# Performance work log

Measured on AMD Instinct MI355X. Metric: run time of the kernel, lower is better.

## Reference

```python
import jax, jax.numpy as jnp
import numpy as np

NODE_SIZE = 100000
DIM = 512
B = 2048
GAMMA = 3.0
LAMB = 20.0
TAU = 8.0


def setup_inputs() -> dict:
    key = jax.random.key(0)
    k1, k2 = jax.random.split(key)
    pairs = jax.random.randint(k1, (B, 2), 0, NODE_SIZE, dtype=jnp.int64 if jax.config.jax_enable_x64 else jnp.int32)
    emb = jax.random.normal(k2, (NODE_SIZE, DIM), dtype=jnp.float32)
    return {"pairs": pairs, "emb": emb}


def _align_loss(pairs, emb):
    l = pairs[:, 0]
    r = pairs[:, 1]
    l_emb = emb[l]                     # [B, D]
    r_emb = emb[r]                     # [B, D]
    pos_dis = jnp.sum(jnp.square(l_emb - r_emb), axis=-1, keepdims=True)  # [B, 1]

    emb_sq = jnp.sum(jnp.square(emb), axis=1)          # [N]

    def squared_dist(A):
        # ||a||^2 + ||b||^2 - 2 a.b  -> [B, N]
        a_sq = jnp.sum(jnp.square(A), axis=1, keepdims=True)
        return a_sq + emb_sq[None, :] - 2.0 * (A @ emb.T)

    l_neg_dis = squared_dist(l_emb)
    r_neg_dis = squared_dist(r_emb)

    # mask = 1 - one_hot(l) - one_hot(r), built without materializing one-hots
    rows = jnp.arange(B)
    mask = jnp.ones((B, NODE_SIZE), dtype=emb.dtype)
    mask = mask.at[rows, l].add(-1.0)
    mask = mask.at[rows, r].add(-1.0)

    def norm_lse(loss):
        loss = loss * mask
        mu = jax.lax.stop_gradient(jnp.mean(loss, axis=-1, keepdims=True))
        sd = jax.lax.stop_gradient(jnp.std(loss, axis=-1, keepdims=True))  # unbiased=False
        loss = (loss - mu) / sd
        return jax.scipy.special.logsumexp(LAMB * loss + TAU, axis=-1)

    l_loss = norm_lse(pos_dis - l_neg_dis + GAMMA)
    r_loss = norm_lse(pos_dis - r_neg_dis + GAMMA)
    return jnp.mean(l_loss + r_loss)


def reference(pairs, emb):
    return _align_loss(pairs, emb)
```

## Files before the change

kernel.cpp:

```cpp
#include <hip/hip_runtime.h>
#include <stdint.h>

#define NODES   100000
#define NPAD    100096
#define DIM     512
#define NPAIR   2048
#define MROWS   4096
#define NB      782
#define GAMMA_F 3.0f
#define LAMB_F  20.0f
#define TAU_F   8.0f
#define SHIFT_F 140.0f

#define TM 128
#define TN 128
#define BK 64

typedef __attribute__((ext_vector_type(8))) short          short8;
typedef __attribute__((ext_vector_type(8))) unsigned short ushort8;
typedef __attribute__((ext_vector_type(4))) float          f32x4;


__device__ __forceinline__ unsigned short f2bf(float f) {
    unsigned u = __float_as_uint(f);
    u += 0x7FFFu + ((u >> 16) & 1u);
    return (unsigned short)(u >> 16);
}
__device__ __forceinline__ float bf2f(unsigned short h) {
    return __uint_as_float(((unsigned)h) << 16);
}

__device__ __forceinline__ void gload_lds16(const void* g, void* l) {
    unsigned lofs = (unsigned)__builtin_amdgcn_readfirstlane((unsigned)(uintptr_t)l);
    auto lp = reinterpret_cast<__attribute__((address_space(3))) unsigned*>(lofs);
    auto gp = (const __attribute__((address_space(1))) unsigned*)g;
    __builtin_amdgcn_global_load_lds(gp, lp, 16, 0, 0);
}


__global__ void convert_stats_kernel(const float* __restrict__ emb,
                                     unsigned short* __restrict__ Ebf,
                                     float* __restrict__ esq,
                                     float* __restrict__ Spart,
                                     float* __restrict__ Tpart,
                                     float* __restrict__ E1part,
                                     float* __restrict__ E2part) {
    __shared__ float Sl[4][512];
    __shared__ float Tl[4][512];
    __shared__ float ew[8];
    const int b = blockIdx.x, t = threadIdx.x;
    const int lane = t & 63, wave = t >> 6;
    const int r0 = b * 196;
    float sacc[8], tacc[8];
    #pragma unroll
    for (int k = 0; k < 8; ++k) { sacc[k] = 0.f; tacc[k] = 0.f; }
    float e1 = 0.f, e2 = 0.f;
    for (int i = 0; i < 49; ++i) {
        const int row = r0 + i * 4 + wave;
        if (row >= NPAD) continue;
        const bool real = row < NODES;
        float v[8];
        float ss = 0.f;
        if (real) {
            const float4* p = (const float4*)(emb + (size_t)row * DIM + lane * 8);
            float4 a = p[0], bb = p[1];
            v[0]=a.x; v[1]=a.y; v[2]=a.z; v[3]=a.w;
            v[4]=bb.x; v[5]=bb.y; v[6]=bb.z; v[7]=bb.w;
            #pragma unroll
            for (int k = 0; k < 8; ++k) ss += v[k] * v[k];
        } else {
            #pragma unroll
            for (int k = 0; k < 8; ++k) v[k] = 0.f;
        }
        #pragma unroll
        for (int o = 1; o < 64; o <<= 1) ss += __shfl_xor(ss, o);
        ushort8 o8;
        float vr[8];
        #pragma unroll
        for (int k = 0; k < 8; ++k) { o8[k] = f2bf(v[k]); vr[k] = bf2f(o8[k]); }
        *(ushort8*)(Ebf + (size_t)row * DIM + lane * 8) = o8;
        if (lane == 0) esq[row] = ss;
        if (real) {
            #pragma unroll
            for (int k = 0; k < 8; ++k) { sacc[k] += vr[k]; tacc[k] += ss * vr[k]; }
            if (lane == 0) { e1 += ss; e2 += ss * ss; }
        }
    }
    #pragma unroll
    for (int k = 0; k < 8; ++k) {
        Sl[wave][lane * 8 + k] = sacc[k];
        Tl[wave][lane * 8 + k] = tacc[k];
    }
    if (lane == 0) { ew[wave] = e1; ew[4 + wave] = e2; }
    __syncthreads();
    #pragma unroll
    for (int kk = 0; kk < 2; ++kk) {
        const int d = 2 * t + kk;
        Spart[(size_t)b * 512 + d] = Sl[0][d] + Sl[1][d] + Sl[2][d] + Sl[3][d];
        Tpart[(size_t)b * 512 + d] = Tl[0][d] + Tl[1][d] + Tl[2][d] + Tl[3][d];
    }
    if (t == 0) E1part[b] = ew[0] + ew[1] + ew[2] + ew[3];
    if (t == 1) E2part[b] = ew[4] + ew[5] + ew[6] + ew[7];
}

__global__ void stats_merge_kernel(const float* __restrict__ Spart,
                                   const float* __restrict__ Tpart,
                                   const float* __restrict__ E1part,
                                   const float* __restrict__ E2part,
                                   float* __restrict__ Svec,
                                   float* __restrict__ Tvec,
                                   double* __restrict__ E12) {
    const int bid = blockIdx.x, t = threadIdx.x;
    if (bid < 32) {
        __shared__ float part[8][32];
        const int col = (bid & 15) * 32 + (t & 31);
        const int seg = t >> 5;
        const float* src = (bid < 16) ? Spart : Tpart;
        float s = 0.f;
        const int b0 = seg * 64;
        for (int b = b0; b < b0 + 64; ++b) s += src[(size_t)b * 512 + col];
        part[seg][t & 31] = s;
        __syncthreads();
        if (t < 32) {
            float r = 0.f;
            #pragma unroll
            for (int g = 0; g < 8; ++g) r += part[g][t];
            const int c2 = (bid & 15) * 32 + t;
            if (bid < 16) Svec[c2] = r; else Tvec[c2] = r;
        }
    } else {
        __shared__ double w[4];
        const float* src = (bid == 32) ? E1part : E2part;
        double s = (double)src[t] + (double)src[t + 256];
        #pragma unroll
        for (int o = 1; o < 64; o <<= 1) s += __shfl_xor(s, o);
        if ((t & 63) == 0) w[t >> 6] = s;
        __syncthreads();
        if (t == 0) E12[bid - 32] = w[0] + w[1] + w[2] + w[3];
    }
}

__global__ void gather_kernel(const int* __restrict__ pairs,
                              const float* __restrict__ emb,
                              unsigned short* __restrict__ Abf,
                              float* __restrict__ cvec,
                              float* __restrict__ posv) {
    const int p    = blockIdx.x;
    const int lane = threadIdx.x;
    const int li = pairs[2 * p], ri = pairs[2 * p + 1];
    const float4* pl = (const float4*)(emb + (size_t)li * DIM + lane * 8);
    const float4* pr = (const float4*)(emb + (size_t)ri * DIM + lane * 8);
    float4 a0 = pl[0], a1 = pl[1];
    float4 b0 = pr[0], b1 = pr[1];
    float la[8] = {a0.x,a0.y,a0.z,a0.w,a1.x,a1.y,a1.z,a1.w};
    float lb[8] = {b0.x,b0.y,b0.z,b0.w,b1.x,b1.y,b1.z,b1.w};
    float sa = 0.f, sb = 0.f, sd = 0.f;
    ushort8 oa, ob;
    #pragma unroll
    for (int i = 0; i < 8; ++i) {
        sa += la[i] * la[i];
        sb += lb[i] * lb[i];
        float d = la[i] - lb[i];
        sd += d * d;
        oa[i] = f2bf(la[i]);
        ob[i] = f2bf(lb[i]);
    }
    *(ushort8*)(Abf + (size_t)p * DIM + lane * 8)            = oa;
    *(ushort8*)(Abf + (size_t)(NPAIR + p) * DIM + lane * 8)  = ob;
    #pragma unroll
    for (int off = 1; off < 64; off <<= 1) {
        sa += __shfl_xor(sa, off);
        sb += __shfl_xor(sb, off);
        sd += __shfl_xor(sd, off);
    }
    if (lane == 0) {
        cvec[p]         = sd - sa + GAMMA_F;
        cvec[NPAIR + p] = sd - sb + GAMMA_F;
        posv[p]         = sd;
    }
}


#define GPAD 520

__launch_bounds__(256, 2)
__global__ void gram_kernel(const unsigned short* __restrict__ Ebf,
                            float* __restrict__ Gpart) {
    __shared__ unsigned short ldsA[16 * GPAD];
    __shared__ unsigned short ldsB[16 * GPAD];
    const int tid  = threadIdx.x;
    const int lane = tid & 63;
    const int wave = tid >> 6;
    const int wx = wave & 1, wy = wave >> 1;
    const int d1base = blockIdx.y * 128;
    const int d2base = blockIdx.x * 128;
    const int bz = blockIdx.z;
    const int r15 = lane & 15, q = lane >> 4;

    f32x4 zero4 = {0.f, 0.f, 0.f, 0.f};
    f32x4 acc[4][4];
    #pragma unroll
    for (int i = 0; i < 4; ++i)
        #pragma unroll
        for (int j = 0; j < 4; ++j) acc[i][j] = zero4;

    for (int jc = bz; jc < NPAD / 64; jc += 32) {
        const int j0 = jc * 64;
        #pragma unroll
        for (int ii = 0; ii < 4; ++ii) {
            const int iss = wave * 4 + ii;
            const int row = iss * 4 + (lane >> 4);
            gload_lds16(Ebf + (size_t)(j0 + row) * DIM + d1base + (lane & 15) * 8,
                        &ldsA[iss * GPAD]);
            gload_lds16(Ebf + (size_t)(j0 + row) * DIM + d2base + (lane & 15) * 8,
                        &ldsB[iss * GPAD]);
        }
        __builtin_amdgcn_s_waitcnt(0);
        __syncthreads();
        #pragma unroll
        for (int h = 0; h < 2; ++h) {
            short8 af[4], bfv[4];
            #pragma unroll
            for (int mt = 0; mt < 4; ++mt) {
                const int m = wy * 64 + mt * 16 + r15;
                #pragma unroll
                for (int i = 0; i < 8; ++i) {
                    const int r = h * 32 + q * 8 + i;
                    af[mt][i] = (short)ldsA[(r >> 2) * GPAD + (r & 3) * 128 + m];
                }
            }
            #pragma unroll
            for (int nt = 0; nt < 4; ++nt) {
                const int n = wx * 64 + nt * 16 + r15;
                #pragma unroll
                for (int i = 0; i < 8; ++i) {
                    const int r = h * 32 + q * 8 + i;
                    bfv[nt][i] = (short)ldsB[(r >> 2) * GPAD + (r & 3) * 128 + n];
                }
            }
            #pragma unroll
            for (int mt = 0; mt < 4; ++mt)
                #pragma unroll
                for (int nt = 0; nt < 4; ++nt)
                    acc[mt][nt] = __builtin_amdgcn_mfma_f32_16x16x32_bf16(
                        af[mt], bfv[nt], acc[mt][nt], 0, 0, 0);
        }
        __syncthreads();
    }
    float* gp = Gpart + (size_t)bz * 512 * 512;
    #pragma unroll
    for (int mt = 0; mt < 4; ++mt)
        #pragma unroll
        for (int r = 0; r < 4; ++r) {
            const int d1 = d1base + wy * 64 + mt * 16 + q * 4 + r;
            #pragma unroll
            for (int nt = 0; nt < 4; ++nt) {
                const int d2 = d2base + wx * 64 + nt * 16 + r15;
                gp[d1 * 512 + d2] = acc[mt][nt][r];
            }
        }
}

__global__ void gram_merge_kernel(const float* __restrict__ Gpart,
                                  float* __restrict__ G) {
    const int idx = blockIdx.x * 256 + threadIdx.x;
    float s = 0.f;
    for (int b = 0; b < 32; ++b) s += Gpart[(size_t)b * 512 * 512 + idx];
    G[idx] = s;
}


__launch_bounds__(256)
__global__ void gu_kernel(const unsigned short* __restrict__ Abf,
                          const float* __restrict__ G,
                          const float* __restrict__ Svec,
                          const float* __restrict__ Tvec,
                          const double* __restrict__ E12,
                          const float* __restrict__ cvec,
                          const float* __restrict__ posv,
                          const int* __restrict__ pairs,
                          float* __restrict__ alpha_v,
                          float* __restrict__ shift_v) {
    __shared__ float u[8][512];
    __shared__ float red[8][3][4];
    const int t = threadIdx.x;
    const int lane = t & 63, wave = t >> 6;
    const int r0 = blockIdx.x * 8;
    #pragma unroll
    for (int p = 0; p < 8; ++p) {
        unsigned pk = *(const unsigned*)(Abf + (size_t)(r0 + p) * DIM + 2 * t);
        u[p][2 * t]     = bf2f((unsigned short)(pk & 0xffffu));
        u[p][2 * t + 1] = bf2f((unsigned short)(pk >> 16));
    }
    __syncthreads();
    float acc0[8], acc1[8];
    #pragma unroll
    for (int p = 0; p < 8; ++p) { acc0[p] = 0.f; acc1[p] = 0.f; }
    for (int d1 = 0; d1 < 512; ++d1) {
        const float2 g = *(const float2*)(G + d1 * 512 + 2 * t);
        #pragma unroll
        for (int p = 0; p < 8; ++p) {
            const float up = u[p][d1];
            acc0[p] += up * g.x;
            acc1[p] += up * g.y;
        }
    }
    const float sv0 = Svec[2 * t], sv1 = Svec[2 * t + 1];
    const float tv0 = Tvec[2 * t], tv1 = Tvec[2 * t + 1];
    #pragma unroll
    for (int p = 0; p < 8; ++p) {
        const float u0 = u[p][2 * t], u1 = u[p][2 * t + 1];
        float pdS = u0 * sv0 + u1 * sv1;
        float pdT = u0 * tv0 + u1 * tv1;
        float pq  = u0 * acc0[p] + u1 * acc1[p];
        #pragma unroll
        for (int off = 1; off < 64; off <<= 1) {
            pdS += __shfl_xor(pdS, off);
            pdT += __shfl_xor(pdT, off);
            pq  += __shfl_xor(pq,  off);
        }
        if (lane == 0) {
            red[p][0][wave] = pdS;
            red[p][1][wave] = pdT;
            red[p][2][wave] = pq;
        }
    }
    __syncthreads();
    if (t < 8) {
        const int p = t;
        const double dS = (double)red[p][0][0] + red[p][0][1] + red[p][0][2] + red[p][0][3];
        const double dT = (double)red[p][1][0] + red[p][1][1] + red[p][1][2] + red[p][1][3];
        const double qq = (double)red[p][2][0] + red[p][2][1] + red[p][2][2] + red[p][2][3];
        const int row = r0 + p;
        const int pp  = row & (NPAIR - 1);
        const double c  = (double)cvec[row];
        const double E1 = E12[0], E2 = E12[1];
        const double N  = (double)NODES;
        double Sx  = N * c + 2.0 * dS - E1;
        double Sxx = (N * c * c - 2.0 * c * E1 + E2) + 4.0 * (c * dS - dT) + 4.0 * qq;
        const int li = pairs[2 * pp], ri = pairs[2 * pp + 1];
        const double pos = (double)posv[pp];
        if (li != ri) {
            const double x1 = pos + (double)GAMMA_F, x2 = (double)GAMMA_F;
            Sx  -= x1 + x2;
            Sxx -= x1 * x1 + x2 * x2;
        } else {
            Sx -= 2.0 * (double)GAMMA_F;
        }
        const double mu  = Sx / N;
        const double var = Sxx / N - mu * mu;
        const double sd  = sqrt(fmax(var, 1e-30));
        const double al  = (double)LAMB_F / sd;
        alpha_v[row] = (float)al;
        shift_v[row] = (float)(al * mu + (double)SHIFT_F);
    }
}


__launch_bounds__(256, 2)
__global__ void gemm_kernel(const unsigned short* __restrict__ Abf,
                            const unsigned short* __restrict__ Ebf,
                            const float* __restrict__ cvec,
                            const float* __restrict__ esq,
                            const int*   __restrict__ pairs,
                            const float* __restrict__ alpha_v,
                            const float* __restrict__ shift_v,
                            float* __restrict__ psum) {
    __shared__ unsigned short ldsA[TM * BK];
    __shared__ unsigned short ldsB[TN * BK];
    __shared__ float red_s[2][TM];
    __shared__ float alsh[TM], csh[TM], cmsh[TM];
    __shared__ int   lish[TM], rish[TM];

    const int tid  = threadIdx.x;
    const int lane = tid & 63;
    const int wave = tid >> 6;
    const int wx = wave & 1;
    const int wy = wave >> 1;

    const int d = blockIdx.x;
    const int j = (d & 7) * 782 + (d >> 3);
    const int nb  = j >> 3;
    const int mpg = j & 7;
    const int n0  = nb * TN;

    const int lrow   = lane >> 3;
    const int lchunk = lane & 7;
    const int r15 = lane & 15;
    const int q   = lane >> 4;

    float eqv[4];
    int   gnv[4];
    #pragma unroll
    for (int nt = 0; nt < 4; ++nt) {
        const int gn = n0 + wx * 64 + nt * 16 + r15;
        gnv[nt] = gn;
        eqv[nt] = esq[gn];
    }

    for (int pg = 0; pg < 4; ++pg) {
        const int m0 = (mpg * 4 + pg) * TM;

        if (tid < TM) {
            const int gm = m0 + tid;
            alsh[tid] = alpha_v[gm];
            csh[tid]  = shift_v[gm];
            cmsh[tid] = cvec[gm];
            const int p = gm & (NPAIR - 1);
            lish[tid] = pairs[2 * p];
            rish[tid] = pairs[2 * p + 1];
        }

        f32x4 zero4 = {0.f, 0.f, 0.f, 0.f};
        f32x4 acc[4][4];
        #pragma unroll
        for (int i = 0; i < 4; ++i)
            #pragma unroll
            for (int jj = 0; jj < 4; ++jj) acc[i][jj] = zero4;

        for (int kt = 0; kt < DIM / BK; ++kt) {
            const int kb = kt * BK;
            #pragma unroll
            for (int jj = 0; jj < 4; ++jj) {
                const int rbase = (wave * 4 + jj) * 8;
                const int row   = rbase + lrow;
                const int gch   = lchunk ^ (row & 7);
                gload_lds16(Abf + ((size_t)(m0 + row) * DIM + kb + gch * 8), &ldsA[rbase * BK]);
                gload_lds16(Ebf + ((size_t)(n0 + row) * DIM + kb + gch * 8), &ldsB[rbase * BK]);
            }
            __builtin_amdgcn_s_waitcnt(0);
            __syncthreads();
            #pragma unroll
            for (int h = 0; h < 2; ++h) {
                short8 af[4], bfr[4];
                #pragma unroll
                for (int mt = 0; mt < 4; ++mt) {
                    int row = wy * 64 + mt * 16 + r15;
                    int c   = (h * 4 + q) ^ (row & 7);
                    af[mt] = *(const short8*)&ldsA[row * BK + c * 8];
                }
                #pragma unroll
                for (int nt = 0; nt < 4; ++nt) {
                    int row = wx * 64 + nt * 16 + r15;
                    int c   = (h * 4 + q) ^ (row & 7);
                    bfr[nt] = *(const short8*)&ldsB[row * BK + c * 8];
                }
                #pragma unroll
                for (int mt = 0; mt < 4; ++mt)
                    #pragma unroll
                    for (int nt = 0; nt < 4; ++nt)
                        acc[mt][nt] = __builtin_amdgcn_mfma_f32_16x16x32_bf16(
                            af[mt], bfr[nt], acc[mt][nt], 0, 0, 0);
            }
            __syncthreads();
        }

        #pragma unroll
        for (int mt = 0; mt < 4; ++mt) {
            #pragma unroll
            for (int r = 0; r < 4; ++r) {
                const int rit = wy * 64 + mt * 16 + q * 4 + r;
                const float cm = cmsh[rit];
                const float al = alsh[rit];
                const float Cc = csh[rit];
                const int li = lish[rit], ri = rish[rit];
                float se = 0.f;
                #pragma unroll
                for (int nt = 0; nt < 4; ++nt) {
                    float xv = cm + 2.0f * acc[mt][nt][r] - eqv[nt];
                    float msk = 1.0f - (float)(gnv[nt] == li) - (float)(gnv[nt] == ri);
                    xv *= msk;
                    float term = __expf(fmaf(al, xv, -Cc));
                    se += (gnv[nt] < NODES) ? term : 0.f;
                }
                #pragma unroll
                for (int o = 1; o < 16; o <<= 1) se += __shfl_xor(se, o);
                if (r15 == 0) red_s[wx][rit] = se;
            }
        }
        __syncthreads();
        if (tid < TM) {
            psum[(size_t)nb * MROWS + m0 + tid] = red_s[0][tid] + red_s[1][tid];
        }
    }
}


__global__ void lse_loss_kernel(const float* __restrict__ psum,
                                float* __restrict__ loss_v) {
    const int row = blockIdx.x * 256 + threadIdx.x;
    float s = 0.f;
    for (int nb = 0; nb < NB; ++nb)
        s += psum[(size_t)nb * MROWS + row];
    loss_v[row] = (TAU_F + SHIFT_F) + logf(s);
}

__global__ void final_kernel(const float* __restrict__ loss_v,
                             float* __restrict__ out) {
    __shared__ double wpart[4];
    int t = threadIdx.x;
    double s = 0.0;
    for (int i = t; i < MROWS; i += 256)
        s += (double)loss_v[i];
    #pragma unroll
    for (int off = 1; off < 64; off <<= 1) s += __shfl_xor(s, off);
    if ((t & 63) == 0) wpart[t >> 6] = s;
    __syncthreads();
    if (t == 0) out[0] = (float)((wpart[0] + wpart[1] + wpart[2] + wpart[3]) / (double)NPAIR);
}


extern "C" void kernel_launch(void* const* d_in, const int* in_sizes, int n_in,
                              void* d_out, int out_size, void* d_ws, size_t ws_size,
                              hipStream_t stream) {
    const int*   pairs = (const int*)d_in[0];
    const float* emb   = (const float*)d_in[1];
    float* out = (float*)d_out;

    char* ws = (char*)d_ws;
    size_t off = 0;
    auto alloc = [&](size_t bytes) -> void* {
        void* p = ws + off;
        off += (bytes + 255) & ~(size_t)255;
        return p;
    };
    unsigned short* Ebf = (unsigned short*)alloc((size_t)NPAD * DIM * 2);
    unsigned short* Abf = (unsigned short*)alloc((size_t)MROWS * DIM * 2);
    float*  esq     = (float*)alloc((size_t)NPAD * 4);
    float*  cvec    = (float*)alloc((size_t)MROWS * 4);
    float*  posv    = (float*)alloc((size_t)NPAIR * 4);
    float*  Spart   = (float*)alloc((size_t)512 * DIM * 4);
    float*  Tpart   = (float*)alloc((size_t)512 * DIM * 4);
    float*  E1part  = (float*)alloc((size_t)512 * 4);
    float*  E2part  = (float*)alloc((size_t)512 * 4);
    float*  Svec    = (float*)alloc((size_t)DIM * 4);
    float*  Tvec    = (float*)alloc((size_t)DIM * 4);
    double* E12     = (double*)alloc(2 * sizeof(double));
    float*  G       = (float*)alloc((size_t)512 * 512 * 4);
    float*  alpha_v = (float*)alloc((size_t)MROWS * 4);
    float*  shift_v = (float*)alloc((size_t)MROWS * 4);
    float*  loss_v  = (float*)alloc((size_t)MROWS * 4);
    char* uni = (char*)alloc((size_t)32 * 512 * 512 * 4);
    float* Gpart = (float*)uni;
    float* psum  = (float*)uni;
    if (off > ws_size) return;

    convert_stats_kernel<<<512, 256, 0, stream>>>(emb, Ebf, esq,
                                                  Spart, Tpart, E1part, E2part);
    stats_merge_kernel<<<34, 256, 0, stream>>>(Spart, Tpart, E1part, E2part,
                                               Svec, Tvec, E12);
    gather_kernel<<<NPAIR, 64, 0, stream>>>(pairs, emb, Abf, cvec, posv);

    gram_kernel<<<dim3(4, 4, 32), 256, 0, stream>>>(Ebf, Gpart);
    gram_merge_kernel<<<1024, 256, 0, stream>>>(Gpart, G);
    gu_kernel<<<MROWS / 8, 256, 0, stream>>>(Abf, G, Svec, Tvec, E12,
                                             cvec, posv, pairs, alpha_v, shift_v);

    gemm_kernel<<<6256, 256, 0, stream>>>(Abf, Ebf, cvec, esq, pairs,
                                          alpha_v, shift_v, psum);
    lse_loss_kernel<<<16, 256, 0, stream>>>(psum, loss_v);
    final_kernel<<<1, 256, 0, stream>>>(loss_v, out);
}
```

Before: 1.093 ms.

## Launch one GEMM block per 128x128 output tile instead of looping four row pages

The fused GEMM+exp kernel previously gave each block one 128-column node tile and looped over four 128-row pages, reusing esq values and using a swizzled block index that grouped blocks by M page. It now launches a 2D grid of 782 x 32 blocks, each computing a single 128x128 tile with no inner page loop and no swizzle. This raises block count and parallelism and drops the per-block serial loop. In exchange the E tile stays in cache less predictably across M pages, and per-block setup and esq loads are repeated four times as often.

```diff
diff --git a/kernel.cpp b/kernel.cpp
--- a/kernel.cpp
+++ b/kernel.cpp
@@ -7,6 +7,7 @@
 #define NPAIR   2048
 #define MROWS   4096
 #define NB      782
+#define MPAGES  32
 #define GAMMA_F 3.0f
 #define LAMB_F  20.0f
 #define TAU_F   8.0f
@@ -377,111 +378,96 @@
     const int wave = tid >> 6;
     const int wx = wave & 1;
     const int wy = wave >> 1;
-
-    const int d = blockIdx.x;
-    const int j = (d & 7) * 782 + (d >> 3);
-    const int nb  = j >> 3;
-    const int mpg = j & 7;
-    const int n0  = nb * TN;
+    const int nb = blockIdx.x;
+    const int n0 = nb * TN;
+    const int m0 = blockIdx.y * TM;
+
+    if (tid < TM) {
+        const int gm = m0 + tid;
+        alsh[tid] = alpha_v[gm];
+        csh[tid]  = shift_v[gm];
+        cmsh[tid] = cvec[gm];
+        const int p = gm & (NPAIR - 1);
+        lish[tid] = pairs[2 * p];
+        rish[tid] = pairs[2 * p + 1];
+    }
+
+    f32x4 zero4 = {0.f, 0.f, 0.f, 0.f};
+    f32x4 acc[4][4];
+    #pragma unroll
+    for (int i = 0; i < 4; ++i)
+        #pragma unroll
+        for (int j = 0; j < 4; ++j) acc[i][j] = zero4;
 
     const int lrow   = lane >> 3;
     const int lchunk = lane & 7;
     const int r15 = lane & 15;
     const int q   = lane >> 4;
 
-    float eqv[4];
-    int   gnv[4];
-    #pragma unroll
-    for (int nt = 0; nt < 4; ++nt) {
-        const int gn = n0 + wx * 64 + nt * 16 + r15;
-        gnv[nt] = gn;
-        eqv[nt] = esq[gn];
-    }
-
-    for (int pg = 0; pg < 4; ++pg) {
-        const int m0 = (mpg * 4 + pg) * TM;
-
-        if (tid < TM) {
-            const int gm = m0 + tid;
-            alsh[tid] = alpha_v[gm];
-            csh[tid]  = shift_v[gm];
-            cmsh[tid] = cvec[gm];
-            const int p = gm & (NPAIR - 1);
-            lish[tid] = pairs[2 * p];
-            rish[tid] = pairs[2 * p + 1];
-        }
-
-        f32x4 zero4 = {0.f, 0.f, 0.f, 0.f};
-        f32x4 acc[4][4];
-        #pragma unroll
-        for (int i = 0; i < 4; ++i)
-            #pragma unroll
-            for (int jj = 0; jj < 4; ++jj) acc[i][jj] = zero4;
-
-        for (int kt = 0; kt < DIM / BK; ++kt) {
-            const int kb = kt * BK;
-            #pragma unroll
-            for (int jj = 0; jj < 4; ++jj) {
-                const int rbase = (wave * 4 + jj) * 8;
-                const int row   = rbase + lrow;
-                const int gch   = lchunk ^ (row & 7);
-                gload_lds16(Abf + ((size_t)(m0 + row) * DIM + kb + gch * 8), &ldsA[rbase * BK]);
-                gload_lds16(Ebf + ((size_t)(n0 + row) * DIM + kb + gch * 8), &ldsB[rbase * BK]);
+    for (int kt = 0; kt < DIM / BK; ++kt) {
+        const int kb = kt * BK;
+        #pragma unroll
+        for (int j = 0; j < 4; ++j) {
+            const int rbase = (wave * 4 + j) * 8;
+            const int row   = rbase + lrow;
+            const int gch   = lchunk ^ (row & 7);
+            gload_lds16(Abf + ((size_t)(m0 + row) * DIM + kb + gch * 8), &ldsA[rbase * BK]);
+            gload_lds16(Ebf + ((size_t)(n0 + row) * DIM + kb + gch * 8), &ldsB[rbase * BK]);
+        }
+        __builtin_amdgcn_s_waitcnt(0);
+        __syncthreads();
+        #pragma unroll
+        for (int h = 0; h < 2; ++h) {
+            short8 af[4], bfr[4];
+            #pragma unroll
+            for (int mt = 0; mt < 4; ++mt) {
+                int row = wy * 64 + mt * 16 + r15;
+                int c   = (h * 4 + q) ^ (row & 7);
+                af[mt] = *(const short8*)&ldsA[row * BK + c * 8];
             }
-            __builtin_amdgcn_s_waitcnt(0);
-            __syncthreads();
-            #pragma unroll
-            for (int h = 0; h < 2; ++h) {
-                short8 af[4], bfr[4];
+            #pragma unroll
+            for (int nt = 0; nt < 4; ++nt) {
+                int row = wx * 64 + nt * 16 + r15;
+                int c   = (h * 4 + q) ^ (row & 7);
+                bfr[nt] = *(const short8*)&ldsB[row * BK + c * 8];
+            }
+            #pragma unroll
+            for (int mt = 0; mt < 4; ++mt)
                 #pragma unroll
-                for (int mt = 0; mt < 4; ++mt) {
-                    int row = wy * 64 + mt * 16 + r15;
-                    int c   = (h * 4 + q) ^ (row & 7);
-                    af[mt] = *(const short8*)&ldsA[row * BK + c * 8];
-                }
-                #pragma unroll
-                for (int nt = 0; nt < 4; ++nt) {
-                    int row = wx * 64 + nt * 16 + r15;
-                    int c   = (h * 4 + q) ^ (row & 7);
-                    bfr[nt] = *(const short8*)&ldsB[row * BK + c * 8];
-                }
-                #pragma unroll
-                for (int mt = 0; mt < 4; ++mt)
-                    #pragma unroll
-                    for (int nt = 0; nt < 4; ++nt)
-                        acc[mt][nt] = __builtin_amdgcn_mfma_f32_16x16x32_bf16(
-                            af[mt], bfr[nt], acc[mt][nt], 0, 0, 0);
+                for (int nt = 0; nt < 4; ++nt)
+                    acc[mt][nt] = __builtin_amdgcn_mfma_f32_16x16x32_bf16(
+                        af[mt], bfr[nt], acc[mt][nt], 0, 0, 0);
+        }
+        __syncthreads();
+    }
+
+    #pragma unroll
+    for (int mt = 0; mt < 4; ++mt) {
+        #pragma unroll
+        for (int r = 0; r < 4; ++r) {
+            const int rit = wy * 64 + mt * 16 + q * 4 + r;
+            const float cm = cmsh[rit];
+            const float al = alsh[rit];
+            const float Cc = csh[rit];
+            const int li = lish[rit], ri = rish[rit];
+            float se = 0.f;
+            #pragma unroll
+            for (int nt = 0; nt < 4; ++nt) {
+                const int gn = n0 + wx * 64 + nt * 16 + r15;
+                float xv = cm + 2.0f * acc[mt][nt][r] - esq[gn];
+                float msk = 1.0f - (float)(gn == li) - (float)(gn == ri);
+                xv *= msk;
+                float term = __expf(fmaf(al, xv, -Cc));
+                se += (gn < NODES) ? term : 0.f;
             }
-            __syncthreads();
-        }
-
-        #pragma unroll
-        for (int mt = 0; mt < 4; ++mt) {
-            #pragma unroll
-            for (int r = 0; r < 4; ++r) {
-                const int rit = wy * 64 + mt * 16 + q * 4 + r;
-                const float cm = cmsh[rit];
-                const float al = alsh[rit];
-                const float Cc = csh[rit];
-                const int li = lish[rit], ri = rish[rit];
-                float se = 0.f;
-                #pragma unroll
-                for (int nt = 0; nt < 4; ++nt) {
-                    float xv = cm + 2.0f * acc[mt][nt][r] - eqv[nt];
-                    float msk = 1.0f - (float)(gnv[nt] == li) - (float)(gnv[nt] == ri);
-                    xv *= msk;
-                    float term = __expf(fmaf(al, xv, -Cc));
-                    se += (gnv[nt] < NODES) ? term : 0.f;
-                }
-                #pragma unroll
-                for (int o = 1; o < 16; o <<= 1) se += __shfl_xor(se, o);
-                if (r15 == 0) red_s[wx][rit] = se;
-            }
-        }
-        __syncthreads();
-        if (tid < TM) {
-            psum[(size_t)nb * MROWS + m0 + tid] = red_s[0][tid] + red_s[1][tid];
-        }
+            #pragma unroll
+            for (int o = 1; o < 16; o <<= 1) se += __shfl_xor(se, o);
+            if (r15 == 0) red_s[wx][rit] = se;
+        }
+    }
+    __syncthreads();
+    if (tid < TM) {
+        psum[(size_t)nb * MROWS + m0 + tid] = red_s[0][tid] + red_s[1][tid];
     }
 }
 
@@ -556,8 +542,8 @@
     gu_kernel<<<MROWS / 8, 256, 0, stream>>>(Abf, G, Svec, Tvec, E12,
                                              cvec, posv, pairs, alpha_v, shift_v);
 
-    gemm_kernel<<<6256, 256, 0, stream>>>(Abf, Ebf, cvec, esq, pairs,
-                                          alpha_v, shift_v, psum);
+    gemm_kernel<<<dim3(NB, MPAGES), 256, 0, stream>>>(Abf, Ebf, cvec, esq, pairs,
+                                                      alpha_v, shift_v, psum);
     lse_loss_kernel<<<16, 256, 0, stream>>>(psum, loss_v);
     final_kernel<<<1, 256, 0, stream>>>(loss_v, out);
 }
```

Result: faster. 979.0 us (-10.5%).
